# Performance work log

Hardware: AMD Instinct MI355X
Metric: run time of the kernel (lower is better)

## Reference

```python
import jax, jax.numpy as jnp
import numpy as np

B = 4096        # batch
T = 365         # encoder sequence length
H = 64          # hidden size
HORIZON = 7


def setup_inputs() -> dict:
    key = jax.random.key(0)
    ks = jax.random.split(key, 16)
    s = 0.05
    w = lambda k, shape: (jax.random.normal(k, shape, dtype=jnp.float32) * s)
    return {
        "x": jax.random.normal(ks[0], (B, T, 1), dtype=jnp.float32),
        "enc_Wih0": w(ks[1], (4 * H, 1)),
        "enc_Whh0": w(ks[2], (4 * H, H)),
        "enc_b0": w(ks[3], (4 * H,)),
        "enc_Wih1": w(ks[4], (4 * H, H)),
        "enc_Whh1": w(ks[5], (4 * H, H)),
        "enc_b1": w(ks[6], (4 * H,)),
        "dec_Wih0": w(ks[7], (4 * H, 1)),
        "dec_Whh0": w(ks[8], (4 * H, H)),
        "dec_b0": w(ks[9], (4 * H,)),
        "dec_Wih1": w(ks[10], (4 * H, H)),
        "dec_Whh1": w(ks[11], (4 * H, H)),
        "dec_b1": w(ks[12], (4 * H,)),
        "fc_W": w(ks[13], (1, H)),
        "fc_b": w(ks[14], (1,)),
    }


def _lstm_cell(xt, h, c, Wih, Whh, b):
    # PyTorch gate order: input, forget, cell(g), output
    gates = xt @ Wih.T + h @ Whh.T + b  # [B, 4H]
    i, f, g, o = jnp.split(gates, 4, axis=-1)
    c_new = jax.nn.sigmoid(f) * c + jax.nn.sigmoid(i) * jnp.tanh(g)
    h_new = jax.nn.sigmoid(o) * jnp.tanh(c_new)
    return h_new, c_new


def _run_layer(seq, Wih, Whh, b):
    # seq: [T, B, in] -> hidden seq [T, B, H], final (h, c)
    bsz = seq.shape[1]
    h0 = jnp.zeros((bsz, H), seq.dtype)
    c0 = jnp.zeros((bsz, H), seq.dtype)

    def step(carry, xt):
        h, c = carry
        h, c = _lstm_cell(xt, h, c, Wih, Whh, b)
        return (h, c), h

    (hF, cF), hs = jax.lax.scan(step, (h0, c0), seq)
    return hs, hF, cF


def reference(x, enc_Wih0, enc_Whh0, enc_b0, enc_Wih1, enc_Whh1, enc_b1,
              dec_Wih0, dec_Whh0, dec_b0, dec_Wih1, dec_Whh1, dec_b1,
              fc_W, fc_b):
    xT = jnp.transpose(x, (1, 0, 2))  # [T, B, 1]
    hs0, h0, c0 = _run_layer(xT, enc_Wih0, enc_Whh0, enc_b0)
    _, h1, c1 = _run_layer(hs0, enc_Wih1, enc_Whh1, enc_b1)

    dec_in = jnp.zeros((x.shape[0], 1), x.dtype)  # [B, 1]
    outs = []
    for _ in range(HORIZON):
        h0, c0 = _lstm_cell(dec_in, h0, c0, dec_Wih0, dec_Whh0, dec_b0)
        h1, c1 = _lstm_cell(h0, h1, c1, dec_Wih1, dec_Whh1, dec_b1)
        pred = h1 @ fc_W.T + fc_b  # [B, 1]
        outs.append(pred)
        dec_in = pred
    return jnp.stack(outs, axis=1)  # [B, HORIZON, 1]
```

## Files before the change

### kernel.cpp

```cpp
#include <hip/hip_runtime.h>


typedef _Float16 f16x8 __attribute__((ext_vector_type(8)));
typedef _Float16 f16x4 __attribute__((ext_vector_type(4)));
typedef float    f32x4 __attribute__((ext_vector_type(4)));
typedef float    f32x2 __attribute__((ext_vector_type(2)));

static constexpr int T_ENC = 365;
static constexpr int HZ    = 7;
static constexpr int BT    = 16;
static constexpr int HPAD  = 72;

static constexpr float LOG2E  = 1.442695040888963f;
static constexpr float SCL_I  = -LOG2E;
static constexpr float SCL_G  = 2.0f * LOG2E;

#if __has_builtin(__builtin_amdgcn_exp2f)
__device__ __forceinline__ float fexp2(float x) { return __builtin_amdgcn_exp2f(x); }
#else
__device__ __forceinline__ float fexp2(float x) { return __exp2f(x); }
#endif
#if __has_builtin(__builtin_amdgcn_rcpf)
__device__ __forceinline__ float frcp(float x) { return __builtin_amdgcn_rcpf(x); }
#else
__device__ __forceinline__ float frcp(float x) { return 1.0f / x; }
#endif

__device__ __forceinline__ f32x4 mm1(f16x8 w, f16x8 a, f32x4 acc) {
  return __builtin_amdgcn_mfma_f32_16x16x32_f16(w, a, acc, 0, 0, 0);
}

__global__ __launch_bounds__(512, 2)
void lstm_fused(const float* __restrict__ x,
                const float* __restrict__ eWih0, const float* __restrict__ eWhh0,
                const float* __restrict__ eb0,
                const float* __restrict__ eWih1, const float* __restrict__ eWhh1,
                const float* __restrict__ eb1,
                const float* __restrict__ dWih0, const float* __restrict__ dWhh0,
                const float* __restrict__ db0,
                const float* __restrict__ dWih1, const float* __restrict__ dWhh1,
                const float* __restrict__ db1,
                const float* __restrict__ fcW, const float* __restrict__ fcb,
                float* __restrict__ out)
{
  __shared__ __align__(16) float    xs[T_ENC * BT];
  __shared__ __align__(16) _Float16 h0s[2][BT * HPAD];
  __shared__ __align__(16) _Float16 h1s[2][BT * HPAD];
  __shared__ __align__(16) float    dins[BT];

  const int tid  = threadIdx.x;
  const int lane = tid & 63;
  const int wv   = tid >> 6;
  const int wg   = wv & 3;
  const int n    = lane & 15;
  const int q    = lane >> 4;
  const int b0g  = blockIdx.x * BT;
  const int nH   = n * HPAD;
  const int cbase = (wg << 4) + (q << 2);

#if __has_builtin(__builtin_amdgcn_s_setprio)
  if (wv >= 4) __builtin_amdgcn_s_setprio(1);
#endif

  for (int i = tid; i < T_ENC * BT; i += 512) {
    int b = i / T_ENC;
    int t = i - b * T_ENC;
    xs[t * BT + b] = x[(b0g + b) * T_ENC + t];
  }
  for (int i = tid; i < 2 * BT * HPAD; i += 512) {
    ((_Float16*)h0s)[i] = (_Float16)0.f;
    ((_Float16*)h1s)[i] = (_Float16)0.f;
  }
  if (tid < BT) dins[tid] = 0.f;

  f16x8 WA[4][2], WB[4][2];
  f32x4 biasq[4], wih0q[4];

  auto gscale = [&](int ti) { return (ti == 2) ? SCL_G : SCL_I; };

  auto cvtrow = [&](const float* p, float s, f16x8& w) {
    #pragma unroll
    for (int j = 0; j < 8; ++j) w[j] = (_Float16)(p[j] * s);
  };
  auto loadA = [&](const float* Wih0_, const float* Whh0_, const float* b0_) {
    #pragma unroll
    for (int ti = 0; ti < 4; ++ti) {
      const float s = gscale(ti);
      const int rw = (ti * 4 + wg) * 16 + n;
      const int rq = (ti * 4 + wg) * 16 + (q << 2);
      #pragma unroll
      for (int rr = 0; rr < 4; ++rr) {
        biasq[ti][rr] = b0_[rq + rr] * s;
        wih0q[ti][rr] = Wih0_[rq + rr] * s;
      }
      #pragma unroll
      for (int kc = 0; kc < 2; ++kc)
        cvtrow(Whh0_ + rw * 64 + kc * 32 + q * 8, s, WA[ti][kc]);
    }
  };
  auto loadB = [&](const float* Wih1_, const float* Whh1_, const float* b1_) {
    #pragma unroll
    for (int ti = 0; ti < 4; ++ti) {
      const float s = gscale(ti);
      const int rw = (ti * 4 + wg) * 16 + n;
      const int rq = (ti * 4 + wg) * 16 + (q << 2);
      #pragma unroll
      for (int rr = 0; rr < 4; ++rr) biasq[ti][rr] = b1_[rq + rr] * s;
      #pragma unroll
      for (int kc = 0; kc < 2; ++kc) {
        cvtrow(Wih1_ + rw * 64 + kc * 32 + q * 8, s, WA[ti][kc]);
        cvtrow(Whh1_ + rw * 64 + kc * 32 + q * 8, s, WB[ti][kc]);
      }
    }
  };

  if (wv < 4) loadA(eWih0, eWhh0, eb0);
  else        loadB(eWih1, eWhh1, eb1);

  f32x2 cp[2] = {{0.f, 0.f}, {0.f, 0.f}};

  auto act2 = [&](f32x2 a0, f32x2 a1, f32x2 a2, f32x2 a3, f32x2& c) -> f32x2 {
    f32x2 ei, ef, eg, eo;
    ei.x = fexp2(a0.x); ei.y = fexp2(a0.y);
    ef.x = fexp2(a1.x); ef.y = fexp2(a1.y);
    eg.x = fexp2(a2.x); eg.y = fexp2(a2.y);
    eo.x = fexp2(a3.x); eo.y = fexp2(a3.y);
    const f32x2 one = {1.f, 1.f};
    f32x2 di = one + ei, df = one + ef, dg = one + eg, dd = one + eo;
    f32x2 dif = di * df;
    f32x2 dic = di * c;
    f32x2 t1  = dif * dg;
    f32x2 nd  = eg * df - df;
    f32x2 pc  = dic * dg;
    f32x2 s   = pc + nd;
    const f32x2 sclg = {SCL_G, SCL_G};
    f32x2 sg  = sclg * s;
    f32x2 R1; R1.x = frcp(t1.x); R1.y = frcp(t1.y);
    c = R1 * s;
    f32x2 ca = R1 * sg;
    const f32x2 cap = {20.f, 20.f};
    ca.x = fminf(ca.x, cap.x); ca.y = fminf(ca.y, cap.y);
    f32x2 ec; ec.x = fexp2(ca.x); ec.y = fexp2(ca.y);
    f32x2 t2 = ec * dd + dd;
    f32x2 nc = ec - one;
    f32x2 R2; R2.x = frcp(t2.x); R2.y = frcp(t2.y);
    return nc * R2;
  };

  auto epilogue = [&](const f32x4* g, _Float16* O) {
    f32x2 h2[2];
    #pragma unroll
    for (int pr = 0; pr < 2; ++pr) {
      f32x2 a0 = {g[0][2 * pr], g[0][2 * pr + 1]};
      f32x2 a1 = {g[1][2 * pr], g[1][2 * pr + 1]};
      f32x2 a2 = {g[2][2 * pr], g[2][2 * pr + 1]};
      f32x2 a3 = {g[3][2 * pr], g[3][2 * pr + 1]};
      h2[pr] = act2(a0, a1, a2, a3, cp[pr]);
    }
    f16x4 hv;
    hv[0] = (_Float16)h2[0].x; hv[1] = (_Float16)h2[0].y;
    hv[2] = (_Float16)h2[1].x; hv[3] = (_Float16)h2[1].y;
    *(f16x4*)(O + nH + cbase) = hv;
  };

  auto stepA = [&](const _Float16* H, _Float16* O, float xb) {
    const _Float16* hp = H + nH;
    f16x8 a0 = *(const f16x8*)(hp + q * 8);
    f16x8 a1 = *(const f16x8*)(hp + 32 + q * 8);
    const f32x4 xbv = {xb, xb, xb, xb};
    f32x4 g[4];
    #pragma unroll
    for (int ti = 0; ti < 4; ++ti) {
      f32x4 ci = biasq[ti] + xbv * wih0q[ti];
      f32x4 a = mm1(WA[ti][0], a0, ci);
      a = mm1(WA[ti][1], a1, a);
      g[ti] = a;
    }
    epilogue(g, O);
  };

  auto stepB = [&](const _Float16* H0, const _Float16* H1, _Float16* O) {
    const _Float16* p0 = H0 + nH;
    const _Float16* p1 = H1 + nH;
    f16x8 b0 = *(const f16x8*)(p0 + q * 8);
    f16x8 b1 = *(const f16x8*)(p0 + 32 + q * 8);
    f16x8 a0 = *(const f16x8*)(p1 + q * 8);
    f16x8 a1 = *(const f16x8*)(p1 + 32 + q * 8);
    f32x4 g[4];
    #pragma unroll
    for (int ti = 0; ti < 4; ++ti) {
      f32x4 a = mm1(WA[ti][0], b0, biasq[ti]);
      a = mm1(WA[ti][1], b1, a);
      a = mm1(WB[ti][0], a0, a);
      a = mm1(WB[ti][1], a1, a);
      g[ti] = a;
    }
    epilogue(g, O);
  };

  __syncthreads();


  float xb_next;
  if (wv < 4) {
    float xb = xs[n];
    stepA(h0s[1], h0s[0], xb);
    xb_next = xs[BT + n];
  }
  __syncthreads();

  for (int s = 1; s <= 363; s += 2) {
    if (wv < 4) {
      stepA(h0s[0], h0s[1], xb_next);
      xb_next = xs[(s + 1) * BT + n];
    } else {
      stepB(h0s[0], h1s[1], h1s[0]);
    }
    __syncthreads();
    if (wv < 4) {
      stepA(h0s[1], h0s[0], xb_next);
      if (s + 2 <= 364)
        xb_next = xs[(s + 2) * BT + n];
    } else {
      stepB(h0s[1], h1s[0], h1s[1]);
    }
    __syncthreads();
  }

  if (wv < 4) loadA(dWih0, dWhh0, db0);
  else        stepB(h0s[0], h1s[1], h1s[0]);
  __syncthreads();

  if (wv >= 4) loadB(dWih1, dWhh1, db1);
  float fcw[16];
  #pragma unroll
  for (int j = 0; j < 16; ++j) fcw[j] = fcW[q * 16 + j];
  const float fcb0 = fcb[0];

  #pragma unroll 1
  for (int hz = 0; hz < HZ; ++hz) {
    const int p = hz & 1;
    if (wv < 4) {
      stepA(h0s[p], h0s[1 - p], dins[n]);
    }
    __syncthreads();
    if (wv >= 4) {
      stepB(h0s[1 - p], h1s[p], h1s[1 - p]);
    }
    __syncthreads();
    if (wv == 0) {
      const _Float16* Hh = h1s[1 - p];
      f16x8 hh0 = *(const f16x8*)(Hh + nH + q * 16);
      f16x8 hh1 = *(const f16x8*)(Hh + nH + q * 16 + 8);
      float pacc = 0.f;
      #pragma unroll
      for (int j = 0; j < 8; ++j) pacc += fcw[j] * (float)hh0[j];
      #pragma unroll
      for (int j = 0; j < 8; ++j) pacc += fcw[8 + j] * (float)hh1[j];
      pacc += __shfl_down(pacc, 32);
      pacc += __shfl_down(pacc, 16);
      if (lane < BT) {
        pacc += fcb0;
        out[(b0g + lane) * HZ + hz] = pacc;
        dins[lane] = pacc;
      }
    }
    __syncthreads();
  }
}

extern "C" void kernel_launch(void* const* d_in, const int* in_sizes, int n_in,
                              void* d_out, int out_size, void* d_ws, size_t ws_size,
                              hipStream_t stream) {
  (void)in_sizes; (void)n_in; (void)d_ws; (void)ws_size; (void)out_size;
  const float* x     = (const float*)d_in[0];
  const float* eWih0 = (const float*)d_in[1];
  const float* eWhh0 = (const float*)d_in[2];
  const float* eb0   = (const float*)d_in[3];
  const float* eWih1 = (const float*)d_in[4];
  const float* eWhh1 = (const float*)d_in[5];
  const float* eb1   = (const float*)d_in[6];
  const float* dWih0 = (const float*)d_in[7];
  const float* dWhh0 = (const float*)d_in[8];
  const float* db0   = (const float*)d_in[9];
  const float* dWih1 = (const float*)d_in[10];
  const float* dWhh1 = (const float*)d_in[11];
  const float* db1   = (const float*)d_in[12];
  const float* fcW   = (const float*)d_in[13];
  const float* fcb   = (const float*)d_in[14];
  float* out = (float*)d_out;

  dim3 grid(4096 / BT);
  dim3 block(512);
  hipLaunchKernelGGL(lstm_fused, grid, block, 0, stream,
                     x, eWih0, eWhh0, eb0, eWih1, eWhh1, eb1,
                     dWih0, dWhh0, db0, dWih1, dWhh1, db1, fcW, fcb, out);
}
```

Before: 314.4 us.

## Move layer-1 input projection to layer-0 waves via shared-memory partials

```diff
diff --git a/kernel.cpp b/kernel.cpp
--- a/kernel.cpp
+++ b/kernel.cpp
@@ -46,6 +46,7 @@
   __shared__ __align__(16) float    xs[T_ENC * BT];
   __shared__ __align__(16) _Float16 h0s[2][BT * HPAD];
   __shared__ __align__(16) _Float16 h1s[2][BT * HPAD];
+  __shared__ __align__(16) float    pp[2][16 * 256];
   __shared__ __align__(16) float    dins[BT];
 
   const int tid  = threadIdx.x;
@@ -57,6 +58,8 @@
   const int b0g  = blockIdx.x * BT;
   const int nH   = n * HPAD;
   const int cbase = (wg << 4) + (q << 2);
+  const int ppswz = (n & 7) << 2;
+  const int ppn   = n << 8;
 
 #if __has_builtin(__builtin_amdgcn_s_setprio)
   if (wv >= 4) __builtin_amdgcn_s_setprio(1);
@@ -73,8 +76,8 @@
   }
   if (tid < BT) dins[tid] = 0.f;
 
-  f16x8 WA[4][2], WB[4][2];
-  f32x4 biasq[4], wih0q[4];
+  f16x8 WA[4][2], WB[4][2], WP[4][2];
+  f32x4 biasq[4], wih0q[4], biasqP[4];
 
   auto gscale = [&](int ti) { return (ti == 2) ? SCL_G : SCL_I; };
 
@@ -98,6 +101,19 @@
         cvtrow(Whh0_ + rw * 64 + kc * 32 + q * 8, s, WA[ti][kc]);
     }
   };
+  auto loadAP = [&](const float* Wih1_, const float* b1_) {
+    #pragma unroll
+    for (int ti = 0; ti < 4; ++ti) {
+      const float s = gscale(ti);
+      const int rw = (ti * 4 + wg) * 16 + n;
+      const int rq = (ti * 4 + wg) * 16 + (q << 2);
+      #pragma unroll
+      for (int rr = 0; rr < 4; ++rr) biasqP[ti][rr] = b1_[rq + rr] * s;
+      #pragma unroll
+      for (int kc = 0; kc < 2; ++kc)
+        cvtrow(Wih1_ + rw * 64 + kc * 32 + q * 8, s, WP[ti][kc]);
+    }
+  };
   auto loadB = [&](const float* Wih1_, const float* Whh1_, const float* b1_) {
     #pragma unroll
     for (int ti = 0; ti < 4; ++ti) {
@@ -114,7 +130,7 @@
     }
   };
 
-  if (wv < 4) loadA(eWih0, eWhh0, eb0);
+  if (wv < 4) { loadA(eWih0, eWhh0, eb0); loadAP(eWih1, eb1); }
   else        loadB(eWih1, eWhh1, eb1);
 
   f32x2 cp[2] = {{0.f, 0.f}, {0.f, 0.f}};
@@ -179,6 +195,58 @@
     epilogue(g, O);
   };
 
+  auto stepAP = [&](const _Float16* H, _Float16* O, float xb, float* ppb) {
+    const _Float16* hp = H + nH;
+    f16x8 a0 = *(const f16x8*)(hp + q * 8);
+    f16x8 a1 = *(const f16x8*)(hp + 32 + q * 8);
+    const f32x4 xbv = {xb, xb, xb, xb};
+    f32x4 g[4];
+    #pragma unroll
+    for (int ti = 0; ti < 4; ++ti) {
+      f32x4 ci = biasq[ti] + xbv * wih0q[ti];
+      f32x4 a = mm1(WA[ti][0], a0, ci);
+      a = mm1(WA[ti][1], a1, a);
+      g[ti] = a;
+    }
+    #pragma unroll
+    for (int ti = 0; ti < 4; ++ti) {
+      f32x4 p = mm1(WP[ti][0], a0, biasqP[ti]);
+      p = mm1(WP[ti][1], a1, p);
+      const int rq = ((ti * 4 + wg) << 4) + (q << 2);
+      *(f32x4*)&ppb[ppn + (rq ^ ppswz)] = p;
+    }
+    epilogue(g, O);
+  };
+
+  auto partialOnly = [&](const _Float16* H, float* ppb) {
+    const _Float16* hp = H + nH;
+    f16x8 a0 = *(const f16x8*)(hp + q * 8);
+    f16x8 a1 = *(const f16x8*)(hp + 32 + q * 8);
+    #pragma unroll
+    for (int ti = 0; ti < 4; ++ti) {
+      f32x4 p = mm1(WP[ti][0], a0, biasqP[ti]);
+      p = mm1(WP[ti][1], a1, p);
+      const int rq = ((ti * 4 + wg) << 4) + (q << 2);
+      *(f32x4*)&ppb[ppn + (rq ^ ppswz)] = p;
+    }
+  };
+
+  auto stepB_enc = [&](const _Float16* H1, const float* ppb, _Float16* O) {
+    const _Float16* p1 = H1 + nH;
+    f16x8 a0 = *(const f16x8*)(p1 + q * 8);
+    f16x8 a1 = *(const f16x8*)(p1 + 32 + q * 8);
+    f32x4 g[4];
+    #pragma unroll
+    for (int ti = 0; ti < 4; ++ti) {
+      const int rq = ((ti * 4 + wg) << 4) + (q << 2);
+      f32x4 ci = *(const f32x4*)&ppb[ppn + (rq ^ ppswz)];
+      f32x4 a = mm1(WB[ti][0], a0, ci);
+      a = mm1(WB[ti][1], a1, a);
+      g[ti] = a;
+    }
+    epilogue(g, O);
+  };
+
   auto stepB = [&](const _Float16* H0, const _Float16* H1, _Float16* O) {
     const _Float16* p0 = H0 + nH;
     const _Float16* p1 = H1 + nH;
@@ -200,35 +268,46 @@
 
   __syncthreads();
 
+  float* pp0 = pp[0];
+  float* pp1 = pp[1];
 
   float xb_next;
   if (wv < 4) {
-    float xb = xs[n];
-    stepA(h0s[1], h0s[0], xb);
+    stepA(h0s[1], h0s[0], xs[n]);
     xb_next = xs[BT + n];
   }
   __syncthreads();
-
-  for (int s = 1; s <= 363; s += 2) {
+  if (wv < 4) {
+    stepAP(h0s[0], h0s[1], xb_next, pp0);
+    xb_next = xs[2 * BT + n];
+  }
+  __syncthreads();
+
+  for (int s = 2; s <= 362; s += 2) {
     if (wv < 4) {
-      stepA(h0s[0], h0s[1], xb_next);
+      stepAP(h0s[1], h0s[0], xb_next, pp1);
       xb_next = xs[(s + 1) * BT + n];
     } else {
-      stepB(h0s[0], h1s[1], h1s[0]);
+      stepB_enc(h1s[1], pp0, h1s[0]);
     }
     __syncthreads();
     if (wv < 4) {
-      stepA(h0s[1], h0s[0], xb_next);
-      if (s + 2 <= 364)
-        xb_next = xs[(s + 2) * BT + n];
+      stepAP(h0s[0], h0s[1], xb_next, pp0);
+      xb_next = xs[(s + 2) * BT + n];
     } else {
-      stepB(h0s[1], h1s[0], h1s[1]);
-    }
-    __syncthreads();
-  }
-
+      stepB_enc(h1s[0], pp1, h1s[1]);
+    }
+    __syncthreads();
+  }
+
+  if (wv < 4) stepAP(h0s[1], h0s[0], xb_next, pp1);
+  else        stepB_enc(h1s[1], pp0, h1s[0]);
+  __syncthreads();
+  if (wv < 4) partialOnly(h0s[0], pp0);
+  else        stepB_enc(h1s[0], pp1, h1s[1]);
+  __syncthreads();
   if (wv < 4) loadA(dWih0, dWhh0, db0);
-  else        stepB(h0s[0], h1s[1], h1s[0]);
+  else        stepB_enc(h1s[1], pp0, h1s[0]);
   __syncthreads();
 
   if (wv >= 4) loadB(dWih1, dWhh1, db1);
```

Measured after the change: 323.5 us. 1.03x slower.

## Replace block barriers with three-wave flag-synchronized LSTM pipeline

Applied to the files above, without the earlier changes.

```diff
diff --git a/kernel.cpp b/kernel.cpp
--- a/kernel.cpp
+++ b/kernel.cpp
@@ -8,6 +8,7 @@
 
 static constexpr int T_ENC = 365;
 static constexpr int HZ    = 7;
+static constexpr int TT    = T_ENC + HZ;
 static constexpr int BT    = 16;
 static constexpr int HPAD  = 72;
 
@@ -30,7 +31,14 @@
   return __builtin_amdgcn_mfma_f32_16x16x32_f16(w, a, acc, 0, 0, 0);
 }
 
-__global__ __launch_bounds__(512, 2)
+__device__ __forceinline__ void fence_lds() {
+  asm volatile("s_waitcnt lgkmcnt(0)" ::: "memory");
+}
+__device__ __forceinline__ void waitge(volatile int* f, int target) {
+  while (*f < target) { }
+}
+
+__global__ __launch_bounds__(192, 1)
 void lstm_fused(const float* __restrict__ x,
                 const float* __restrict__ eWih0, const float* __restrict__ eWhh0,
                 const float* __restrict__ eb0,
@@ -44,80 +52,81 @@
                 float* __restrict__ out)
 {
   __shared__ __align__(16) float    xs[T_ENC * BT];
-  __shared__ __align__(16) _Float16 h0s[2][BT * HPAD];
-  __shared__ __align__(16) _Float16 h1s[2][BT * HPAD];
+  __shared__ __align__(16) _Float16 h0r[2][BT * HPAD];
+  __shared__ __align__(16) _Float16 h1r[2][BT * HPAD];
+  __shared__ __align__(16) float    pp[2][16 * 256];
   __shared__ __align__(16) float    dins[BT];
+  __shared__ int flg[4];
 
   const int tid  = threadIdx.x;
   const int lane = tid & 63;
   const int wv   = tid >> 6;
-  const int wg   = wv & 3;
   const int n    = lane & 15;
   const int q    = lane >> 4;
   const int b0g  = blockIdx.x * BT;
   const int nH   = n * HPAD;
-  const int cbase = (wg << 4) + (q << 2);
-
-#if __has_builtin(__builtin_amdgcn_s_setprio)
-  if (wv >= 4) __builtin_amdgcn_s_setprio(1);
-#endif
-
-  for (int i = tid; i < T_ENC * BT; i += 512) {
+  const int ppswz = (n & 7) << 2;
+  const int ppn   = n << 8;
+
+  for (int i = tid; i < T_ENC * BT; i += 192) {
     int b = i / T_ENC;
     int t = i - b * T_ENC;
     xs[t * BT + b] = x[(b0g + b) * T_ENC + t];
   }
-  for (int i = tid; i < 2 * BT * HPAD; i += 512) {
-    ((_Float16*)h0s)[i] = (_Float16)0.f;
-    ((_Float16*)h1s)[i] = (_Float16)0.f;
+  for (int i = tid; i < 2 * BT * HPAD; i += 192) {
+    ((_Float16*)h0r)[i] = (_Float16)0.f;
+    ((_Float16*)h1r)[i] = (_Float16)0.f;
   }
   if (tid < BT) dins[tid] = 0.f;
-
-  f16x8 WA[4][2], WB[4][2];
-  f32x4 biasq[4], wih0q[4];
+  if (tid < 4)  flg[tid] = 0;
+
+  f16x8 WA[4][4][2];
+  f32x4 biasq[4][4], wih0q[4][4];
+  f32x2 cp[4][2] = {};
 
   auto gscale = [&](int ti) { return (ti == 2) ? SCL_G : SCL_I; };
-
   auto cvtrow = [&](const float* p, float s, f16x8& w) {
     #pragma unroll
     for (int j = 0; j < 8; ++j) w[j] = (_Float16)(p[j] * s);
   };
-  auto loadA = [&](const float* Wih0_, const float* Whh0_, const float* b0_) {
-    #pragma unroll
-    for (int ti = 0; ti < 4; ++ti) {
-      const float s = gscale(ti);
-      const int rw = (ti * 4 + wg) * 16 + n;
-      const int rq = (ti * 4 + wg) * 16 + (q << 2);
-      #pragma unroll
-      for (int rr = 0; rr < 4; ++rr) {
-        biasq[ti][rr] = b0_[rq + rr] * s;
-        wih0q[ti][rr] = Wih0_[rq + rr] * s;
-      }
-      #pragma unroll
-      for (int kc = 0; kc < 2; ++kc)
-        cvtrow(Whh0_ + rw * 64 + kc * 32 + q * 8, s, WA[ti][kc]);
-    }
-  };
-  auto loadB = [&](const float* Wih1_, const float* Whh1_, const float* b1_) {
-    #pragma unroll
-    for (int ti = 0; ti < 4; ++ti) {
-      const float s = gscale(ti);
-      const int rw = (ti * 4 + wg) * 16 + n;
-      const int rq = (ti * 4 + wg) * 16 + (q << 2);
-      #pragma unroll
-      for (int rr = 0; rr < 4; ++rr) biasq[ti][rr] = b1_[rq + rr] * s;
-      #pragma unroll
-      for (int kc = 0; kc < 2; ++kc) {
-        cvtrow(Wih1_ + rw * 64 + kc * 32 + q * 8, s, WA[ti][kc]);
-        cvtrow(Whh1_ + rw * 64 + kc * 32 + q * 8, s, WB[ti][kc]);
-      }
-    }
-  };
-
-  if (wv < 4) loadA(eWih0, eWhh0, eb0);
-  else        loadB(eWih1, eWhh1, eb1);
-
-  f32x2 cp[2] = {{0.f, 0.f}, {0.f, 0.f}};
+  auto loadFrags = [&](const float* W_) {
+    #pragma unroll
+    for (int wb = 0; wb < 4; ++wb)
+      #pragma unroll
+      for (int ti = 0; ti < 4; ++ti) {
+        const float s = gscale(ti);
+        const int rw = (ti * 4 + wb) * 16 + n;
+        #pragma unroll
+        for (int kc = 0; kc < 2; ++kc)
+          cvtrow(W_ + rw * 64 + kc * 32 + q * 8, s, WA[wb][ti][kc]);
+      }
+  };
+  auto loadBias = [&](const float* b_) {
+    #pragma unroll
+    for (int wb = 0; wb < 4; ++wb)
+      #pragma unroll
+      for (int ti = 0; ti < 4; ++ti) {
+        const float s = gscale(ti);
+        const int rq = (ti * 4 + wb) * 16 + (q << 2);
+        #pragma unroll
+        for (int rr = 0; rr < 4; ++rr) biasq[wb][ti][rr] = b_[rq + rr] * s;
+      }
+  };
+  auto loadWih0 = [&](const float* W_) {
+    #pragma unroll
+    for (int wb = 0; wb < 4; ++wb)
+      #pragma unroll
+      for (int ti = 0; ti < 4; ++ti) {
+        const float s = gscale(ti);
+        const int rq = (ti * 4 + wb) * 16 + (q << 2);
+        #pragma unroll
+        for (int rr = 0; rr < 4; ++rr) wih0q[wb][ti][rr] = W_[rq + rr] * s;
+      }
+  };
+
+  if (wv == 0)      { loadFrags(eWhh0); loadBias(eb0); loadWih0(eWih0); }
+  else if (wv == 1) { loadFrags(eWhh1); }
+  else              { loadFrags(eWih1); loadBias(eb1); }
 
   auto act2 = [&](f32x2 a0, f32x2 a1, f32x2 a2, f32x2 a3, f32x2& c) -> f32x2 {
     f32x2 ei, ef, eg, eo;
@@ -147,7 +156,7 @@
     return nc * R2;
   };
 
-  auto epilogue = [&](const f32x4* g, _Float16* O) {
+  auto epilog_wb = [&](const f32x4* g, f32x2* cpw, _Float16* O, int wb) {
     f32x2 h2[2];
     #pragma unroll
     for (int pr = 0; pr < 2; ++pr) {
@@ -155,117 +164,124 @@
       f32x2 a1 = {g[1][2 * pr], g[1][2 * pr + 1]};
       f32x2 a2 = {g[2][2 * pr], g[2][2 * pr + 1]};
       f32x2 a3 = {g[3][2 * pr], g[3][2 * pr + 1]};
-      h2[pr] = act2(a0, a1, a2, a3, cp[pr]);
+      h2[pr] = act2(a0, a1, a2, a3, cpw[pr]);
     }
     f16x4 hv;
     hv[0] = (_Float16)h2[0].x; hv[1] = (_Float16)h2[0].y;
     hv[2] = (_Float16)h2[1].x; hv[3] = (_Float16)h2[1].y;
-    *(f16x4*)(O + nH + cbase) = hv;
-  };
-
-  auto stepA = [&](const _Float16* H, _Float16* O, float xb) {
-    const _Float16* hp = H + nH;
-    f16x8 a0 = *(const f16x8*)(hp + q * 8);
-    f16x8 a1 = *(const f16x8*)(hp + 32 + q * 8);
-    const f32x4 xbv = {xb, xb, xb, xb};
-    f32x4 g[4];
-    #pragma unroll
-    for (int ti = 0; ti < 4; ++ti) {
-      f32x4 ci = biasq[ti] + xbv * wih0q[ti];
-      f32x4 a = mm1(WA[ti][0], a0, ci);
-      a = mm1(WA[ti][1], a1, a);
-      g[ti] = a;
+    *(f16x4*)(O + nH + (wb << 4) + (q << 2)) = hv;
+  };
+
+  __syncthreads();
+
+  if (wv == 0) {
+    #pragma unroll 1
+    for (int t = 0; t < TT; ++t) {
+      if (t == T_ENC) { loadFrags(dWhh0); loadBias(db0); loadWih0(dWih0); }
+      float xb;
+      if (t < T_ENC) {
+        xb = xs[t * BT + n];
+      } else {
+        waitge((volatile int*)&flg[3], t - T_ENC);
+        xb = dins[n];
+      }
+      if (t >= 2) waitge((volatile int*)&flg[1], t - 1);
+      const _Float16* hp = h0r[(t + 1) & 1] + nH;
+      _Float16* O = h0r[t & 1];
+      f16x8 a0 = *(const f16x8*)(hp + q * 8);
+      f16x8 a1 = *(const f16x8*)(hp + 32 + q * 8);
+      const f32x4 xbv = {xb, xb, xb, xb};
+      #pragma unroll
+      for (int wb = 0; wb < 4; ++wb) {
+        f32x4 g[4];
+        #pragma unroll
+        for (int ti = 0; ti < 4; ++ti) {
+          f32x4 ci = biasq[wb][ti] + xbv * wih0q[wb][ti];
+          f32x4 a = mm1(WA[wb][ti][0], a0, ci);
+          a = mm1(WA[wb][ti][1], a1, a);
+          g[ti] = a;
+        }
+        epilog_wb(g, cp[wb], O, wb);
+      }
+      fence_lds();
+      if (lane == 0) *(volatile int*)&flg[0] = t + 1;
     }
-    epilogue(g, O);
-  };
-
-  auto stepB = [&](const _Float16* H0, const _Float16* H1, _Float16* O) {
-    const _Float16* p0 = H0 + nH;
-    const _Float16* p1 = H1 + nH;
-    f16x8 b0 = *(const f16x8*)(p0 + q * 8);
-    f16x8 b1 = *(const f16x8*)(p0 + 32 + q * 8);
-    f16x8 a0 = *(const f16x8*)(p1 + q * 8);
-    f16x8 a1 = *(const f16x8*)(p1 + 32 + q * 8);
-    f32x4 g[4];
-    #pragma unroll
-    for (int ti = 0; ti < 4; ++ti) {
-      f32x4 a = mm1(WA[ti][0], b0, biasq[ti]);
-      a = mm1(WA[ti][1], b1, a);
-      a = mm1(WB[ti][0], a0, a);
-      a = mm1(WB[ti][1], a1, a);
-      g[ti] = a;
+  } else if (wv == 2) {
+    #pragma unroll 1
+    for (int t = 0; t < TT; ++t) {
+      if (t == T_ENC) { loadFrags(dWih1); loadBias(db1); }
+      waitge((volatile int*)&flg[0], t + 1);
+      if (t >= 2) waitge((volatile int*)&flg[2], t - 1);
+      const _Float16* hp = h0r[t & 1] + nH;
+      float* ppb = pp[t & 1];
+      f16x8 a0 = *(const f16x8*)(hp + q * 8);
+      f16x8 a1 = *(const f16x8*)(hp + 32 + q * 8);
+      #pragma unroll
+      for (int wb = 0; wb < 4; ++wb) {
+        #pragma unroll
+        for (int ti = 0; ti < 4; ++ti) {
+          f32x4 p = mm1(WA[wb][ti][0], a0, biasq[wb][ti]);
+          p = mm1(WA[wb][ti][1], a1, p);
+          const int rq = ((ti * 4 + wb) << 4) + (q << 2);
+          *(f32x4*)&ppb[ppn + (rq ^ ppswz)] = p;
+        }
+      }
+      fence_lds();
+      if (lane == 0) *(volatile int*)&flg[1] = t + 1;
     }
-    epilogue(g, O);
-  };
-
-  __syncthreads();
-
-
-  float xb_next;
-  if (wv < 4) {
-    float xb = xs[n];
-    stepA(h0s[1], h0s[0], xb);
-    xb_next = xs[BT + n];
-  }
-  __syncthreads();
-
-  for (int s = 1; s <= 363; s += 2) {
-    if (wv < 4) {
-      stepA(h0s[0], h0s[1], xb_next);
-      xb_next = xs[(s + 1) * BT + n];
-    } else {
-      stepB(h0s[0], h1s[1], h1s[0]);
+  } else {
+    float fcw[16];
+    float fcb0 = 0.f;
+    #pragma unroll 1
+    for (int t = 0; t < TT; ++t) {
+      if (t == T_ENC) {
+        loadFrags(dWhh1);
+        #pragma unroll
+        for (int j = 0; j < 16; ++j) fcw[j] = fcW[q * 16 + j];
+        fcb0 = fcb[0];
+      }
+      waitge((volatile int*)&flg[1], t + 1);
+      const _Float16* hp = h1r[(t + 1) & 1] + nH;
+      _Float16* O = h1r[t & 1];
+      const float* ppb = pp[t & 1];
+      f16x8 a0 = *(const f16x8*)(hp + q * 8);
+      f16x8 a1 = *(const f16x8*)(hp + 32 + q * 8);
+      #pragma unroll
+      for (int wb = 0; wb < 4; ++wb) {
+        f32x4 g[4];
+        #pragma unroll
+        for (int ti = 0; ti < 4; ++ti) {
+          const int rq = ((ti * 4 + wb) << 4) + (q << 2);
+          f32x4 ci = *(const f32x4*)&ppb[ppn + (rq ^ ppswz)];
+          f32x4 a = mm1(WA[wb][ti][0], a0, ci);
+          a = mm1(WA[wb][ti][1], a1, a);
+          g[ti] = a;
+        }
+        epilog_wb(g, cp[wb], O, wb);
+      }
+      fence_lds();
+      if (lane == 0) *(volatile int*)&flg[2] = t + 1;
+      if (t >= T_ENC) {
+        const int hz = t - T_ENC;
+        const _Float16* Hh = h1r[t & 1];
+        f16x8 hh0 = *(const f16x8*)(Hh + nH + q * 16);
+        f16x8 hh1 = *(const f16x8*)(Hh + nH + q * 16 + 8);
+        float pacc = 0.f;
+        #pragma unroll
+        for (int j = 0; j < 8; ++j) pacc += fcw[j] * (float)hh0[j];
+        #pragma unroll
+        for (int j = 0; j < 8; ++j) pacc += fcw[8 + j] * (float)hh1[j];
+        pacc += __shfl_down(pacc, 32);
+        pacc += __shfl_down(pacc, 16);
+        if (lane < BT) {
+          pacc += fcb0;
+          out[(b0g + lane) * HZ + hz] = pacc;
+          dins[lane] = pacc;
+        }
+        fence_lds();
+        if (lane == 0) *(volatile int*)&flg[3] = hz + 1;
+      }
     }
-    __syncthreads();
-    if (wv < 4) {
-      stepA(h0s[1], h0s[0], xb_next);
-      if (s + 2 <= 364)
-        xb_next = xs[(s + 2) * BT + n];
-    } else {
-      stepB(h0s[1], h1s[0], h1s[1]);
-    }
-    __syncthreads();
-  }
-
-  if (wv < 4) loadA(dWih0, dWhh0, db0);
-  else        stepB(h0s[0], h1s[1], h1s[0]);
-  __syncthreads();
-
-  if (wv >= 4) loadB(dWih1, dWhh1, db1);
-  float fcw[16];
-  #pragma unroll
-  for (int j = 0; j < 16; ++j) fcw[j] = fcW[q * 16 + j];
-  const float fcb0 = fcb[0];
-
-  #pragma unroll 1
-  for (int hz = 0; hz < HZ; ++hz) {
-    const int p = hz & 1;
-    if (wv < 4) {
-      stepA(h0s[p], h0s[1 - p], dins[n]);
-    }
-    __syncthreads();
-    if (wv >= 4) {
-      stepB(h0s[1 - p], h1s[p], h1s[1 - p]);
-    }
-    __syncthreads();
-    if (wv == 0) {
-      const _Float16* Hh = h1s[1 - p];
-      f16x8 hh0 = *(const f16x8*)(Hh + nH + q * 16);
-      f16x8 hh1 = *(const f16x8*)(Hh + nH + q * 16 + 8);
-      float pacc = 0.f;
-      #pragma unroll
-      for (int j = 0; j < 8; ++j) pacc += fcw[j] * (float)hh0[j];
-      #pragma unroll
-      for (int j = 0; j < 8; ++j) pacc += fcw[8 + j] * (float)hh1[j];
-      pacc += __shfl_down(pacc, 32);
-      pacc += __shfl_down(pacc, 16);
-      if (lane < BT) {
-        pacc += fcb0;
-        out[(b0g + lane) * HZ + hz] = pacc;
-        dins[lane] = pacc;
-      }
-    }
-    __syncthreads();
   }
 }
 
@@ -291,7 +307,7 @@
   float* out = (float*)d_out;
 
   dim3 grid(4096 / BT);
-  dim3 block(512);
+  dim3 block(192);
   hipLaunchKernelGGL(lstm_fused, grid, block, 0, stream,
                      x, eWih0, eWhh0, eb0, eWih1, eWhh1, eb1,
                      dWih0, dWhh0, db0, dWih1, dWhh1, db1, fcW, fcb, out);
```

Result: slower. 698.5 us (+122.2%).
